# Performance work log

Hardware: AMD Instinct MI355X
Metric: run time of the kernel (lower is better)

Reference implementation:

```python
import jax, jax.numpy as jnp
import numpy as np

TEMPERATURE = 0.07

def _l2_normalize(x):
    # F.normalize(x, dim=1): x / max(||x||, eps)
    n = jnp.linalg.norm(x, axis=1, keepdims=True)
    return x / jnp.maximum(n, 1e-12)

def setup_inputs() -> dict:
    key = jax.random.key(0)
    k1, k2, k3, k4 = jax.random.split(key, 4)
    B, D, N = 4096, 256, 131072
    anchor = jax.random.normal(k1, (B, D), dtype=jnp.float32)
    positive = jax.random.normal(k2, (B, D), dtype=jnp.float32)
    negatives = jax.random.normal(k3, (N, D), dtype=jnp.float32)
    neg_batch_indices = jnp.sort(jax.random.randint(k4, (N,), 0, B, dtype=jnp.int32))
    return {"anchor": anchor, "positive": positive, "negatives": negatives,
            "neg_batch_indices": neg_batch_indices}

def reference(anchor, positive, negatives, neg_batch_indices):
    B = anchor.shape[0]
    a = _l2_normalize(anchor)            # [B, D]
    p = _l2_normalize(positive)          # [B, D]
    n = _l2_normalize(negatives)         # [N, D]
    pos_sim = jnp.sum(a * p, axis=1) / TEMPERATURE                     # [B]
    # only sims between a negative and its owning anchor are ever used ->
    # gather instead of the dense [B, N] matmul the torch loop masks.
    neg_sim = jnp.sum(a[neg_batch_indices] * n, axis=1) / TEMPERATURE  # [N]
    seg_max = jax.ops.segment_max(neg_sim, neg_batch_indices, num_segments=B)  # -inf for empty
    counts = jax.ops.segment_sum(jnp.ones_like(neg_sim), neg_batch_indices, num_segments=B)
    m = jax.lax.stop_gradient(jnp.maximum(pos_sim, seg_max))           # [B], finite
    sum_exp = jnp.exp(pos_sim - m) + jax.ops.segment_sum(
        jnp.exp(neg_sim - m[neg_batch_indices]), neg_batch_indices, num_segments=B)
    loss_i = -pos_sim + m + jnp.log(sum_exp)                           # [B]
    loss_i = jnp.where(counts > 0, loss_i, 0.0)  # torch skips empty groups
    loss = jnp.sum(loss_i) / B
    correct = (counts > 0) & (pos_sim > seg_max)  # (pos > all negs), empty -> skipped
    accuracy = jnp.mean(correct.astype(jnp.float32))
    return loss, accuracy
```

## Files before the change

kernel.cpp:

```cpp
#include <hip/hip_runtime.h>
#include <math.h>

#define TEMP_INV (1.0f / 0.07f)

typedef float vf4 __attribute__((ext_vector_type(4)));

__device__ __forceinline__ float wave_reduce_sum(float v) {
    #pragma unroll
    for (int off = 32; off; off >>= 1) v += __shfl_down(v, off);
    return v;
}

__device__ __forceinline__ float wave_reduce_max(float v) {
    #pragma unroll
    for (int off = 32; off; off >>= 1) v = fmaxf(v, __shfl_down(v, off));
    return v;
}

__global__ void k_stats(const float* __restrict__ A, const float* __restrict__ P,
                        const float* __restrict__ Ng, const int* __restrict__ idx,
                        float* __restrict__ inv_na, float* __restrict__ pos_sim,
                        float* __restrict__ raw, int* __restrict__ seg_start,
                        int B, int N, int rowBlocks, int segBlocks, int negBlocks) {
    int bid  = (int)blockIdx.x;
    int wib  = threadIdx.x >> 6;
    int lane = threadIdx.x & 63;

    if (bid < rowBlocks) {
        int b = bid * 4 + wib;
        if (b >= B) return;
        const float4 a = reinterpret_cast<const float4*>(A + (size_t)b * 256)[lane];
        const float4 p = reinterpret_cast<const float4*>(P + (size_t)b * 256)[lane];
        float sa = a.x * a.x + a.y * a.y + a.z * a.z + a.w * a.w;
        float sp = p.x * p.x + p.y * p.y + p.z * p.z + p.w * p.w;
        float dp = a.x * p.x + a.y * p.y + a.z * p.z + a.w * p.w;
        sa = wave_reduce_sum(sa);
        sp = wave_reduce_sum(sp);
        dp = wave_reduce_sum(dp);
        if (lane == 0) {
            float ia = 1.0f / fmaxf(sqrtf(sa), 1e-12f);
            float ip = 1.0f / fmaxf(sqrtf(sp), 1e-12f);
            inv_na[b]  = ia;
            pos_sim[b] = dp * ia * ip * TEMP_INV;
        }
    } else if (bid < rowBlocks + segBlocks) {
        int t0 = (bid - rowBlocks) * 256 + (int)threadIdx.x;
        int nthreads = segBlocks * 256;
        for (int j = t0; j <= N; j += nthreads) {
            if (j == 0) {
                int c = idx[0];
                for (int v = 0; v <= c; ++v) seg_start[v] = 0;
            } else if (j < N) {
                int prev = idx[j - 1], cur = idx[j];
                for (int v = prev + 1; v <= cur; ++v) seg_start[v] = j;
            } else {
                int prev = idx[N - 1];
                for (int v = prev + 1; v <= B; ++v) seg_start[v] = N;
            }
        }
    } else {
        int wave    = (bid - rowBlocks - segBlocks) * 4 + wib;
        int nwaves  = negBlocks * 4;
        int nchunks = N >> 2;
        for (int chunk = wave; chunk < nchunks; chunk += nwaves) {
            int j0 = chunk * 4;
            int b0 = idx[j0], b1 = idx[j0 + 1], b2 = idx[j0 + 2], b3 = idx[j0 + 3];
            const vf4 n0 = __builtin_nontemporal_load(
                reinterpret_cast<const vf4*>(Ng + (size_t)j0 * 256) + lane);
            const vf4 n1 = __builtin_nontemporal_load(
                reinterpret_cast<const vf4*>(Ng + (size_t)(j0 + 1) * 256) + lane);
            const vf4 n2 = __builtin_nontemporal_load(
                reinterpret_cast<const vf4*>(Ng + (size_t)(j0 + 2) * 256) + lane);
            const vf4 n3 = __builtin_nontemporal_load(
                reinterpret_cast<const vf4*>(Ng + (size_t)(j0 + 3) * 256) + lane);
            const float4 a0 = reinterpret_cast<const float4*>(A + (size_t)b0 * 256)[lane];
            const float4 a1 = reinterpret_cast<const float4*>(A + (size_t)b1 * 256)[lane];
            const float4 a2 = reinterpret_cast<const float4*>(A + (size_t)b2 * 256)[lane];
            const float4 a3 = reinterpret_cast<const float4*>(A + (size_t)b3 * 256)[lane];

            float sn0 = n0.x*n0.x + n0.y*n0.y + n0.z*n0.z + n0.w*n0.w;
            float sn1 = n1.x*n1.x + n1.y*n1.y + n1.z*n1.z + n1.w*n1.w;
            float sn2 = n2.x*n2.x + n2.y*n2.y + n2.z*n2.z + n2.w*n2.w;
            float sn3 = n3.x*n3.x + n3.y*n3.y + n3.z*n3.z + n3.w*n3.w;
            float dp0 = a0.x*n0.x + a0.y*n0.y + a0.z*n0.z + a0.w*n0.w;
            float dp1 = a1.x*n1.x + a1.y*n1.y + a1.z*n1.z + a1.w*n1.w;
            float dp2 = a2.x*n2.x + a2.y*n2.y + a2.z*n2.z + a2.w*n2.w;
            float dp3 = a3.x*n3.x + a3.y*n3.y + a3.z*n3.z + a3.w*n3.w;

            sn0 = wave_reduce_sum(sn0); dp0 = wave_reduce_sum(dp0);
            sn1 = wave_reduce_sum(sn1); dp1 = wave_reduce_sum(dp1);
            sn2 = wave_reduce_sum(sn2); dp2 = wave_reduce_sum(dp2);
            sn3 = wave_reduce_sum(sn3); dp3 = wave_reduce_sum(dp3);

            if (lane == 0) {
                raw[j0]     = dp0 * (1.0f / fmaxf(sqrtf(sn0), 1e-12f)) * TEMP_INV;
                raw[j0 + 1] = dp1 * (1.0f / fmaxf(sqrtf(sn1), 1e-12f)) * TEMP_INV;
                raw[j0 + 2] = dp2 * (1.0f / fmaxf(sqrtf(sn2), 1e-12f)) * TEMP_INV;
                raw[j0 + 3] = dp3 * (1.0f / fmaxf(sqrtf(sn3), 1e-12f)) * TEMP_INV;
            }
        }
    }
}

__global__ void k_seg(const float* __restrict__ raw, const int* __restrict__ seg_start,
                      const float* __restrict__ inv_na, const float* __restrict__ pos_sim,
                      float* __restrict__ loss_i, float* __restrict__ corr, int B) {
    int b = (int)blockIdx.x * 4 + (threadIdx.x >> 6);
    int lane = threadIdx.x & 63;
    if (b >= B) return;

    int s = seg_start[b];
    int e = seg_start[b + 1];

    float ps = pos_sim[b];
    float ia = inv_na[b];

    float l_val = 0.0f, c_val = 0.0f;
    if (e > s) {
        const float M = TEMP_INV;
        float mx = -INFINITY, se = 0.0f;
        for (int j = s + lane; j < e; j += 64) {
            float t = raw[j] * ia;
            mx = fmaxf(mx, t);
            se += expf(t - M);
        }
        mx = wave_reduce_max(mx);
        se = wave_reduce_sum(se);
        mx = __shfl(mx, 0);
        se = __shfl(se, 0);
        l_val = -ps + M + logf(se + expf(ps - M));
        c_val = (ps > mx) ? 1.0f : 0.0f;
    }
    if (lane == 0) { loss_i[b] = l_val; corr[b] = c_val; }
}

__global__ void k_final(const float* __restrict__ loss_i, const float* __restrict__ corr,
                        float* __restrict__ out, int B) {
    __shared__ float sl[256];
    __shared__ float sc[256];
    float l = 0.0f, c = 0.0f;
    for (int i = threadIdx.x; i < B; i += 256) { l += loss_i[i]; c += corr[i]; }
    sl[threadIdx.x] = l; sc[threadIdx.x] = c;
    __syncthreads();
    for (int s = 128; s; s >>= 1) {
        if ((int)threadIdx.x < s) {
            sl[threadIdx.x] += sl[threadIdx.x + s];
            sc[threadIdx.x] += sc[threadIdx.x + s];
        }
        __syncthreads();
    }
    if (threadIdx.x == 0) {
        out[0] = sl[0] / (float)B;
        out[1] = sc[0] / (float)B;
    }
}

extern "C" void kernel_launch(void* const* d_in, const int* in_sizes, int n_in,
                              void* d_out, int out_size, void* d_ws, size_t ws_size,
                              hipStream_t stream) {
    const float* anchor    = (const float*)d_in[0];
    const float* positive  = (const float*)d_in[1];
    const float* negatives = (const float*)d_in[2];
    const int*   idx       = (const int*)d_in[3];

    const int D = 256;
    const int B = in_sizes[0] / D;
    const int N = in_sizes[2] / D;

    float* ws        = (float*)d_ws;
    float* raw       = ws;
    float* inv_na    = ws + N;
    float* pos_sim   = ws + N + B;
    float* loss_i    = ws + N + 2 * B;
    float* corr      = ws + N + 3 * B;
    int*   seg_start = (int*)(ws + N + 4 * B);

    float* out = (float*)d_out;

    int rowBlocks = (B + 3) / 4;
    int segBlocks = 64;
    int negBlocks = 2048;

    k_stats<<<rowBlocks + segBlocks + negBlocks, 256, 0, stream>>>(
        anchor, positive, negatives, idx, inv_na, pos_sim, raw, seg_start,
        B, N, rowBlocks, segBlocks, negBlocks);

    k_seg<<<(B + 3) / 4, 256, 0, stream>>>(raw, seg_start, inv_na, pos_sim,
                                           loss_i, corr, B);

    k_final<<<1, 256, 0, stream>>>(loss_i, corr, out, B);
}
```

Measured before the change: 38.14 us.

## Merge block roles into uniform waves and use transposed shuffle reductions

Removes the specialised block roles so that every wave does a positive-row job, a share of segment-start work, and a grid-stride share of negative chunks. The four anchor indices are read with one int4 load and made scalar with readfirstlane, and when all four negatives share one anchor the anchor row is loaded only once. Eight separate wave reductions are replaced by a butterfly merge that folds several values into a single shuffle tree. The final reduction switches to 1024 threads with wave-level shuffles. The aim is to cut shuffle instruction count and redundant anchor loads in a kernel that is mostly bound by memory bandwidth.

```diff
diff --git a/kernel.cpp b/kernel.cpp
--- a/kernel.cpp
+++ b/kernel.cpp
@@ -17,36 +17,45 @@
     return v;
 }
 
-__global__ void k_stats(const float* __restrict__ A, const float* __restrict__ P,
-                        const float* __restrict__ Ng, const int* __restrict__ idx,
-                        float* __restrict__ inv_na, float* __restrict__ pos_sim,
-                        float* __restrict__ raw, int* __restrict__ seg_start,
-                        int B, int N, int rowBlocks, int segBlocks, int negBlocks) {
-    int bid  = (int)blockIdx.x;
-    int wib  = threadIdx.x >> 6;
-    int lane = threadIdx.x & 63;
-
-    if (bid < rowBlocks) {
-        int b = bid * 4 + wib;
-        if (b >= B) return;
+__device__ __forceinline__ float merge2(float lo, float hi, int span, int lane) {
+    float a = lo + __shfl_xor(lo, span);
+    float b = hi + __shfl_xor(hi, span);
+    return (lane & span) ? b : a;
+}
+
+__global__ void k_main(const float* __restrict__ A, const float* __restrict__ P,
+                       const float* __restrict__ Ng, const int* __restrict__ idx,
+                       float* __restrict__ inv_na, float* __restrict__ pos_sim,
+                       float* __restrict__ raw, int* __restrict__ seg_start,
+                       int B, int N) {
+    const int bid  = (int)blockIdx.x;
+    const int wib  = threadIdx.x >> 6;
+    const int lane = threadIdx.x & 63;
+    const int wave = bid * 4 + wib;
+    const int nwaves = (int)gridDim.x * 4;
+
+    if (wave < B) {
+        int b = wave;
         const float4 a = reinterpret_cast<const float4*>(A + (size_t)b * 256)[lane];
         const float4 p = reinterpret_cast<const float4*>(P + (size_t)b * 256)[lane];
         float sa = a.x * a.x + a.y * a.y + a.z * a.z + a.w * a.w;
         float sp = p.x * p.x + p.y * p.y + p.z * p.z + p.w * p.w;
-        float dp = a.x * p.x + a.y * p.y + a.z * p.z + a.w * p.w;
+        float dq = a.x * p.x + a.y * p.y + a.z * p.z + a.w * p.w;
         sa = wave_reduce_sum(sa);
         sp = wave_reduce_sum(sp);
-        dp = wave_reduce_sum(dp);
+        dq = wave_reduce_sum(dq);
         if (lane == 0) {
             float ia = 1.0f / fmaxf(sqrtf(sa), 1e-12f);
             float ip = 1.0f / fmaxf(sqrtf(sp), 1e-12f);
             inv_na[b]  = ia;
-            pos_sim[b] = dp * ia * ip * TEMP_INV;
-        }
-    } else if (bid < rowBlocks + segBlocks) {
-        int t0 = (bid - rowBlocks) * 256 + (int)threadIdx.x;
-        int nthreads = segBlocks * 256;
-        for (int j = t0; j <= N; j += nthreads) {
+            pos_sim[b] = dq * ia * ip * TEMP_INV;
+        }
+    }
+
+    {
+        int t = bid * 256 + (int)threadIdx.x;
+        int stride = (int)gridDim.x * 256;
+        for (int j = t; j <= N; j += stride) {
             if (j == 0) {
                 int c = idx[0];
                 for (int v = 0; v <= c; ++v) seg_start[v] = 0;
@@ -58,46 +67,61 @@
                 for (int v = prev + 1; v <= B; ++v) seg_start[v] = N;
             }
         }
-    } else {
-        int wave    = (bid - rowBlocks - segBlocks) * 4 + wib;
-        int nwaves  = negBlocks * 4;
-        int nchunks = N >> 2;
-        for (int chunk = wave; chunk < nchunks; chunk += nwaves) {
-            int j0 = chunk * 4;
-            int b0 = idx[j0], b1 = idx[j0 + 1], b2 = idx[j0 + 2], b3 = idx[j0 + 3];
-            const vf4 n0 = __builtin_nontemporal_load(
-                reinterpret_cast<const vf4*>(Ng + (size_t)j0 * 256) + lane);
-            const vf4 n1 = __builtin_nontemporal_load(
-                reinterpret_cast<const vf4*>(Ng + (size_t)(j0 + 1) * 256) + lane);
-            const vf4 n2 = __builtin_nontemporal_load(
-                reinterpret_cast<const vf4*>(Ng + (size_t)(j0 + 2) * 256) + lane);
-            const vf4 n3 = __builtin_nontemporal_load(
-                reinterpret_cast<const vf4*>(Ng + (size_t)(j0 + 3) * 256) + lane);
-            const float4 a0 = reinterpret_cast<const float4*>(A + (size_t)b0 * 256)[lane];
-            const float4 a1 = reinterpret_cast<const float4*>(A + (size_t)b1 * 256)[lane];
-            const float4 a2 = reinterpret_cast<const float4*>(A + (size_t)b2 * 256)[lane];
-            const float4 a3 = reinterpret_cast<const float4*>(A + (size_t)b3 * 256)[lane];
-
-            float sn0 = n0.x*n0.x + n0.y*n0.y + n0.z*n0.z + n0.w*n0.w;
-            float sn1 = n1.x*n1.x + n1.y*n1.y + n1.z*n1.z + n1.w*n1.w;
-            float sn2 = n2.x*n2.x + n2.y*n2.y + n2.z*n2.z + n2.w*n2.w;
-            float sn3 = n3.x*n3.x + n3.y*n3.y + n3.z*n3.z + n3.w*n3.w;
-            float dp0 = a0.x*n0.x + a0.y*n0.y + a0.z*n0.z + a0.w*n0.w;
-            float dp1 = a1.x*n1.x + a1.y*n1.y + a1.z*n1.z + a1.w*n1.w;
-            float dp2 = a2.x*n2.x + a2.y*n2.y + a2.z*n2.z + a2.w*n2.w;
-            float dp3 = a3.x*n3.x + a3.y*n3.y + a3.z*n3.z + a3.w*n3.w;
-
-            sn0 = wave_reduce_sum(sn0); dp0 = wave_reduce_sum(dp0);
-            sn1 = wave_reduce_sum(sn1); dp1 = wave_reduce_sum(dp1);
-            sn2 = wave_reduce_sum(sn2); dp2 = wave_reduce_sum(dp2);
-            sn3 = wave_reduce_sum(sn3); dp3 = wave_reduce_sum(dp3);
-
-            if (lane == 0) {
-                raw[j0]     = dp0 * (1.0f / fmaxf(sqrtf(sn0), 1e-12f)) * TEMP_INV;
-                raw[j0 + 1] = dp1 * (1.0f / fmaxf(sqrtf(sn1), 1e-12f)) * TEMP_INV;
-                raw[j0 + 2] = dp2 * (1.0f / fmaxf(sqrtf(sn2), 1e-12f)) * TEMP_INV;
-                raw[j0 + 3] = dp3 * (1.0f / fmaxf(sqrtf(sn3), 1e-12f)) * TEMP_INV;
-            }
+    }
+
+    const int nchunks = N >> 2;
+    const float4* A4 = reinterpret_cast<const float4*>(A);
+    for (int chunk = wave; chunk < nchunks; chunk += nwaves) {
+        int j0 = chunk << 2;
+        int4 bi = *reinterpret_cast<const int4*>(idx + j0);
+        int b0 = __builtin_amdgcn_readfirstlane(bi.x);
+        int b1 = __builtin_amdgcn_readfirstlane(bi.y);
+        int b2 = __builtin_amdgcn_readfirstlane(bi.z);
+        int b3 = __builtin_amdgcn_readfirstlane(bi.w);
+
+        const vf4 n0 = __builtin_nontemporal_load(
+            reinterpret_cast<const vf4*>(Ng + (size_t)j0 * 256) + lane);
+        const vf4 n1 = __builtin_nontemporal_load(
+            reinterpret_cast<const vf4*>(Ng + (size_t)(j0 + 1) * 256) + lane);
+        const vf4 n2 = __builtin_nontemporal_load(
+            reinterpret_cast<const vf4*>(Ng + (size_t)(j0 + 2) * 256) + lane);
+        const vf4 n3 = __builtin_nontemporal_load(
+            reinterpret_cast<const vf4*>(Ng + (size_t)(j0 + 3) * 256) + lane);
+
+        float4 a0 = A4[(size_t)b0 * 64 + lane];
+        float4 a1, a2, a3;
+        if (b3 == b0) {
+            a1 = a0; a2 = a0; a3 = a0;
+        } else {
+            a1 = A4[(size_t)b1 * 64 + lane];
+            a2 = A4[(size_t)b2 * 64 + lane];
+            a3 = A4[(size_t)b3 * 64 + lane];
+        }
+
+        float sn0 = n0.x*n0.x + n0.y*n0.y + n0.z*n0.z + n0.w*n0.w;
+        float dp0 = a0.x*n0.x + a0.y*n0.y + a0.z*n0.z + a0.w*n0.w;
+        float sn1 = n1.x*n1.x + n1.y*n1.y + n1.z*n1.z + n1.w*n1.w;
+        float dp1 = a1.x*n1.x + a1.y*n1.y + a1.z*n1.z + a1.w*n1.w;
+        float sn2 = n2.x*n2.x + n2.y*n2.y + n2.z*n2.z + n2.w*n2.w;
+        float dp2 = a2.x*n2.x + a2.y*n2.y + a2.z*n2.z + a2.w*n2.w;
+        float sn3 = n3.x*n3.x + n3.y*n3.y + n3.z*n3.z + n3.w*n3.w;
+        float dp3 = a3.x*n3.x + a3.y*n3.y + a3.z*n3.z + a3.w*n3.w;
+
+        float nv0 = merge2(sn0, sn2, 32, lane);
+        float nv1 = merge2(dp0, dp2, 32, lane);
+        float nv2 = merge2(sn1, sn3, 32, lane);
+        float nv3 = merge2(dp1, dp3, 32, lane);
+        float m0  = merge2(nv0, nv2, 16, lane);
+        float m1  = merge2(nv1, nv3, 16, lane);
+        float f   = merge2(m0,  m1,   8, lane);
+        f += __shfl_xor(f, 4);
+        f += __shfl_xor(f, 2);
+        f += __shfl_xor(f, 1);
+
+        float fdp = __shfl_down(f, 8);
+        if ((lane & 15) == 0) {
+            int r = lane >> 4;
+            raw[j0 + r] = fdp * (1.0f / fmaxf(sqrtf(f), 1e-12f)) * TEMP_INV;
         }
     }
 }
@@ -136,22 +160,24 @@
 
 __global__ void k_final(const float* __restrict__ loss_i, const float* __restrict__ corr,
                         float* __restrict__ out, int B) {
-    __shared__ float sl[256];
-    __shared__ float sc[256];
+    __shared__ float sl[16];
+    __shared__ float sc[16];
+    int tid = (int)threadIdx.x, lane = tid & 63, wid = tid >> 6;
     float l = 0.0f, c = 0.0f;
-    for (int i = threadIdx.x; i < B; i += 256) { l += loss_i[i]; c += corr[i]; }
-    sl[threadIdx.x] = l; sc[threadIdx.x] = c;
+    for (int i = tid; i < B; i += 1024) { l += loss_i[i]; c += corr[i]; }
+    l = wave_reduce_sum(l);
+    c = wave_reduce_sum(c);
+    if (lane == 0) { sl[wid] = l; sc[wid] = c; }
     __syncthreads();
-    for (int s = 128; s; s >>= 1) {
-        if ((int)threadIdx.x < s) {
-            sl[threadIdx.x] += sl[threadIdx.x + s];
-            sc[threadIdx.x] += sc[threadIdx.x + s];
-        }
-        __syncthreads();
-    }
-    if (threadIdx.x == 0) {
-        out[0] = sl[0] / (float)B;
-        out[1] = sc[0] / (float)B;
+    if (wid == 0) {
+        float lv = (lane < 16) ? sl[lane] : 0.0f;
+        float cv = (lane < 16) ? sc[lane] : 0.0f;
+        lv = wave_reduce_sum(lv);
+        cv = wave_reduce_sum(cv);
+        if (lane == 0) {
+            out[0] = lv / (float)B;
+            out[1] = cv / (float)B;
+        }
     }
 }
 
@@ -177,16 +203,11 @@
 
     float* out = (float*)d_out;
 
-    int rowBlocks = (B + 3) / 4;
-    int segBlocks = 64;
-    int negBlocks = 2048;
-
-    k_stats<<<rowBlocks + segBlocks + negBlocks, 256, 0, stream>>>(
-        anchor, positive, negatives, idx, inv_na, pos_sim, raw, seg_start,
-        B, N, rowBlocks, segBlocks, negBlocks);
+    k_main<<<2048, 256, 0, stream>>>(anchor, positive, negatives, idx,
+                                     inv_na, pos_sim, raw, seg_start, B, N);
 
     k_seg<<<(B + 3) / 4, 256, 0, stream>>>(raw, seg_start, inv_na, pos_sim,
                                            loss_i, corr, B);
 
-    k_final<<<1, 256, 0, stream>>>(loss_i, corr, out, B);
-}
+    k_final<<<1, 1024, 0, stream>>>(loss_i, corr, out, B);
+}
```

Result: faster. 34.19 us (-10.3%).
